# Kernel optimization log

Hardware: AMD Instinct MI355X
Metric: run time of the kernel (lower is better)

## Reference

```python
import jax, jax.numpy as jnp
import numpy as np


def setup_inputs() -> dict:
    key = jax.random.key(0)
    k1, k2, k3, k4 = jax.random.split(key, 4)
    B, Cin, Cout, H, W = 4, 256, 256, 96, 96
    x = jax.random.normal(k1, (B, Cin, H, W), dtype=jnp.float32)
    offset = jax.random.normal(k2, (B, 18, H, W), dtype=jnp.float32)
    mask = jax.random.uniform(k3, (B, 9, H, W), dtype=jnp.float32)
    weight = jax.random.normal(k4, (Cout, Cin, 3, 3), dtype=jnp.float32) * 0.05
    gamma = jnp.ones((Cout,), dtype=jnp.float32)
    beta = jnp.zeros((Cout,), dtype=jnp.float32)
    return {"x": x, "offset": offset, "mask": mask, "weight": weight, "gamma": gamma, "beta": beta}


def reference(x, offset, mask, weight, gamma, beta):
    # Modulated deformable conv v2 (3x3, stride 1, pad 1, no bias) + GroupNorm(8) + ReLU
    B, C, H, W = x.shape
    O = weight.shape[0]
    K = 9
    xh = jnp.transpose(x, (0, 2, 3, 1))  # [B,H,W,C]
    ky, kx = jnp.meshgrid(jnp.arange(3), jnp.arange(3), indexing="ij")
    ky = ky.reshape(1, K, 1, 1).astype(x.dtype)
    kx = kx.reshape(1, K, 1, 1).astype(x.dtype)
    off = offset.reshape(B, K, 2, H, W)  # (dy, dx) per kernel tap, row-major taps
    gy = jnp.arange(H, dtype=x.dtype).reshape(1, 1, H, 1)
    gx = jnp.arange(W, dtype=x.dtype).reshape(1, 1, 1, W)
    py = gy + ky - 1.0 + off[:, :, 0]  # [B,K,H,W] sampling y
    px = gx + kx - 1.0 + off[:, :, 1]  # [B,K,H,W] sampling x
    y0 = jnp.floor(py)
    x0 = jnp.floor(px)
    wy = py - y0
    wx = px - x0
    y0i = y0.astype(jnp.int32)
    x0i = x0.astype(jnp.int32)
    bidx = jnp.arange(B).reshape(B, 1, 1, 1)

    def gather(yi, xi):
        valid = ((yi >= 0) & (yi < H) & (xi >= 0) & (xi < W)).astype(x.dtype)
        v = xh[bidx, jnp.clip(yi, 0, H - 1), jnp.clip(xi, 0, W - 1)]  # [B,K,H,W,C]
        return v * valid[..., None]

    val = (gather(y0i, x0i) * ((1 - wy) * (1 - wx))[..., None]
           + gather(y0i, x0i + 1) * ((1 - wy) * wx)[..., None]
           + gather(y0i + 1, x0i) * (wy * (1 - wx))[..., None]
           + gather(y0i + 1, x0i + 1) * (wy * wx)[..., None])
    val = val * mask[..., None]  # modulation, [B,K,H,W,C]
    out = jnp.einsum("bkhwc,ock->bohw", val, weight.reshape(O, C, K))
    # GroupNorm with 8 groups, eps=1e-5 (affine)
    G = 8
    og = out.reshape(B, G, O // G, H, W)
    mu = og.mean(axis=(2, 3, 4), keepdims=True)
    var = og.var(axis=(2, 3, 4), keepdims=True)
    og = (og - mu) * jax.lax.rsqrt(var + 1e-5)
    out = og.reshape(B, O, H, W) * gamma.reshape(1, O, 1, 1) + beta.reshape(1, O, 1, 1)
    return jax.nn.relu(out)
```

## Files before the change

### kernel.cpp

```cpp
#include <hip/hip_runtime.h>
#include <hip/hip_bf16.h>
#include <stdint.h>

typedef __attribute__((ext_vector_type(4))) float f32x4;
typedef __attribute__((ext_vector_type(8))) short s16x8;
typedef __attribute__((ext_vector_type(4))) unsigned int u32x4;
typedef unsigned short u16;
typedef unsigned int u32;

#define B_ 4
#define C_ 256
#define O_ 256
#define H_ 96
#define W_ 96
#define HW_ (H_*W_)
#define M_ (B_*HW_)

static __device__ __forceinline__ float asf(u32 u){
    union { u32 u; float f; } x; x.u = u; return x.f;
}
static __device__ __forceinline__ u16 f2bf(float f){
    union { float f; u32 u; } x; x.f = f;
    u32 u = x.u;
    u32 r = (u + 0x7fffu + ((u >> 16) & 1u)) >> 16;
    return (u16)r;
}
static __device__ __forceinline__ u32 blerp_pack(u32 q00, u32 q01, u32 q10, u32 q11,
                                                 float w00, float w01, float w10, float w11)
{
    float f0 = asf(q00 << 16) * w00 + asf(q01 << 16) * w01
             + asf(q10 << 16) * w10 + asf(q11 << 16) * w11;
    float f1 = asf(q00) * w00 + asf(q01) * w01 + asf(q10) * w10 + asf(q11) * w11;
    float2 fp; fp.x = f0; fp.y = f1;
    __hip_bfloat162 hb = __float22bfloat162_rn(fp);
    union { __hip_bfloat162 h; u32 u; } cv; cv.h = hb;
    return cv.u;
}

struct TapCtx {
    float w00, w01, w10, w11;
    u32 o00, o01, o10, o11;
};

static __device__ __forceinline__ TapCtx tap_setup(
    int tap, int b, int h, int w, int hw,
    const float* __restrict__ off, const float* __restrict__ msk)
{
    TapCtx t;
    float dy = off[(size_t)(b * 18 + 2 * tap) * HW_ + hw];
    float dx = off[(size_t)(b * 18 + 2 * tap + 1) * HW_ + hw];
    float mk = msk[(size_t)(b * 9 + tap) * HW_ + hw];
    float py = (float)(h + tap / 3 - 1) + dy;
    float px = (float)(w + tap % 3 - 1) + dx;
    float fy = floorf(py), fx = floorf(px);
    float wy = py - fy, wx = px - fx;
    int y0 = (int)fy, x0 = (int)fx;
    int y1 = y0 + 1, x1 = x0 + 1;
    float w00 = (1.f - wy) * (1.f - wx) * mk;
    float w01 = (1.f - wy) * wx * mk;
    float w10 = wy * (1.f - wx) * mk;
    float w11 = wy * wx * mk;
    if (y0 < 0 || y0 >= H_) { w00 = 0.f; w01 = 0.f; }
    if (y1 < 0 || y1 >= H_) { w10 = 0.f; w11 = 0.f; }
    if (x0 < 0 || x0 >= W_) { w00 = 0.f; w10 = 0.f; }
    if (x1 < 0 || x1 >= W_) { w01 = 0.f; w11 = 0.f; }
    int cy0 = min(max(y0, 0), H_ - 1), cy1 = min(max(y1, 0), H_ - 1);
    int cx0 = min(max(x0, 0), W_ - 1), cx1 = min(max(x1, 0), W_ - 1);
    u32 rb = (u32)b * (u32)(HW_ * C_);
    t.o00 = rb + ((u32)(cy0 * W_ + cx0)) * C_;
    t.o01 = rb + ((u32)(cy0 * W_ + cx1)) * C_;
    t.o10 = rb + ((u32)(cy1 * W_ + cx0)) * C_;
    t.o11 = rb + ((u32)(cy1 * W_ + cx1)) * C_;
    t.w00 = w00; t.w01 = w01; t.w10 = w10; t.w11 = w11;
    return t;
}

__global__ __launch_bounds__(256) void transpose_x(const float* __restrict__ x,
                                                   u16* __restrict__ xT)
{
    __shared__ float t[32][33];
    int tid = threadIdx.x;
    int tx = tid & 31, ty = tid >> 5;
    int bi = blockIdx.x;
    int w0 = (bi % 3) * 32;
    int c0 = ((bi / 3) % 8) * 32;
    int bh = bi / 24;
    int b = bh / H_, h = bh - b * H_;
    #pragma unroll
    for (int r = 0; r < 4; ++r){
        int c = c0 + ty + r * 8;
        t[ty + r * 8][tx] = x[(size_t)(b * C_ + c) * HW_ + h * W_ + w0 + tx];
    }
    __syncthreads();
    #pragma unroll
    for (int r = 0; r < 4; ++r){
        int w = w0 + ty + r * 8;
        xT[((size_t)(b * H_ + h) * W_ + w) * C_ + c0 + tx] = f2bf(t[tx][ty + r * 8]);
    }
}

__global__ __launch_bounds__(256) void pack_w(const float* __restrict__ wt,
                                              u16* __restrict__ w3)
{
    int n = blockIdx.x * 256 + threadIdx.x;
    int o = n / 2304;
    int rem = n - o * 2304;
    int c = rem / 9;
    int tap = rem - c * 9;
    int kidx = tap * 256 + c;
    w3[(size_t)(kidx >> 3) * 2048 + o * 8 + (kidx & 7)] = f2bf(wt[n]);
}

__global__ __launch_bounds__(512, 4) void dcn_main(
    const float* __restrict__ off, const float* __restrict__ msk,
    const u16* __restrict__ xT, const u16* __restrict__ w3,
    float* __restrict__ convOut, float* __restrict__ stats)
{
    __shared__ u16 At[2][64 * 256];
    int tid = threadIdx.x;
    int lane = tid & 63;
    int wv = tid >> 6;
    int l15 = lane & 15;
    int g = lane >> 4;

    int bid = blockIdx.x;
    int tile = (bid & 7) * 72 + (bid >> 3);
    int b = tile / 144;
    int t = tile - b * 144;
    int ty_ = t / 12, tx_ = t - ty_ * 12;
    int py0 = ty_ * 8, px0 = tx_ * 8;

    f32x4 acc[4][2];
    #pragma unroll
    for (int i = 0; i < 4; ++i)
        #pragma unroll
        for (int q = 0; q < 2; ++q)
            acc[i][q] = (f32x4){0.f, 0.f, 0.f, 0.f};

    int p = tid >> 3;
    int k = tid & 7;
    int h = py0 + (p >> 3);
    int w = px0 + (p & 7);
    int hw = h * W_ + w;

    {
        TapCtx tp = tap_setup(0, b, h, w, hw, off, msk);
        #pragma unroll
        for (int i = 0; i < 4; ++i){
            int ck = k + i * 8;
            int c = ck * 8;
            u32x4 q00 = *(const u32x4*)(xT + tp.o00 + c);
            u32x4 q01 = *(const u32x4*)(xT + tp.o01 + c);
            u32x4 q10 = *(const u32x4*)(xT + tp.o10 + c);
            u32x4 q11 = *(const u32x4*)(xT + tp.o11 + c);
            u32x4 outv;
            #pragma unroll
            for (int j = 0; j < 4; ++j)
                outv[j] = blerp_pack(q00[j], q01[j], q10[j], q11[j],
                                     tp.w00, tp.w01, tp.w10, tp.w11);
            u32 boff = (u32)(p * 512) + (u32)((ck ^ (p & 15)) << 4);
            *(u32x4*)((char*)&At[0][0] + boff) = outv;
        }
    }
    __syncthreads();

    int cur = 0;
    for (int tap = 0; tap < 9; ++tap){
        bool pre = (tap < 8);
        TapCtx tn;
        u32x4 s00, s01, s10, s11;
        if (pre){
            tn = tap_setup(tap + 1, b, h, w, hw, off, msk);
            int c = k * 8;
            s00 = *(const u32x4*)(xT + tn.o00 + c);
            s01 = *(const u32x4*)(xT + tn.o01 + c);
            s10 = *(const u32x4*)(xT + tn.o10 + c);
            s11 = *(const u32x4*)(xT + tn.o11 + c);
        }
        const char* Ac = (const char*)&At[cur][0];
        char* An = (char*)&At[cur ^ 1][0];

        #pragma unroll
        for (int half = 0; half < 4; ++half){
            __builtin_amdgcn_s_setprio(1);
            #pragma unroll
            for (int s = 0; s < 2; ++s){
                int step = half * 2 + s;
                int ck = step * 4 + g;
                s16x8 a[4];
                #pragma unroll
                for (int i = 0; i < 4; ++i){
                    int r = i * 16 + l15;
                    u32 boff = (u32)(r * 512) + (u32)((ck ^ (r & 15)) << 4);
                    a[i] = *(const s16x8*)(Ac + boff);
                }
                const u16* wrow = w3 + (size_t)(tap * 32 + step * 4 + g) * 2048
                                + (size_t)(wv * 32 + l15) * 8;
                s16x8 b0 = *(const s16x8*)(wrow);
                s16x8 b1 = *(const s16x8*)(wrow + 128);
                #pragma unroll
                for (int i = 0; i < 4; ++i){
                    acc[i][0] = __builtin_amdgcn_mfma_f32_16x16x32_bf16(a[i], b0, acc[i][0], 0, 0, 0);
                    acc[i][1] = __builtin_amdgcn_mfma_f32_16x16x32_bf16(a[i], b1, acc[i][1], 0, 0, 0);
                }
            }
            __builtin_amdgcn_s_setprio(0);

            if (pre){
                int ck = k + half * 8;
                u32x4 outv;
                #pragma unroll
                for (int j = 0; j < 4; ++j)
                    outv[j] = blerp_pack(s00[j], s01[j], s10[j], s11[j],
                                         tn.w00, tn.w01, tn.w10, tn.w11);
                u32 boff = (u32)(p * 512) + (u32)((ck ^ (p & 15)) << 4);
                *(u32x4*)(An + boff) = outv;
                if (half < 3){
                    int c = (k + (half + 1) * 8) * 8;
                    s00 = *(const u32x4*)(xT + tn.o00 + c);
                    s01 = *(const u32x4*)(xT + tn.o01 + c);
                    s10 = *(const u32x4*)(xT + tn.o10 + c);
                    s11 = *(const u32x4*)(xT + tn.o11 + c);
                }
            }
        }
        __syncthreads();
        cur ^= 1;
    }

    float s0 = 0.f, s20 = 0.f;
    size_t mbase = (size_t)b * HW_;
    #pragma unroll
    for (int i = 0; i < 4; ++i){
        #pragma unroll
        for (int q = 0; q < 2; ++q){
            int oc = wv * 32 + q * 16 + l15;
            #pragma unroll
            for (int j = 0; j < 4; ++j){
                float v = acc[i][q][j];
                int pp = i * 16 + g * 4 + j;
                int mr_hw = (py0 + (pp >> 3)) * W_ + px0 + (pp & 7);
                convOut[(mbase + mr_hw) * 256 + oc] = v;
                s0 += v; s20 += v * v;
            }
        }
    }
    #pragma unroll
    for (int d = 32; d; d >>= 1){
        s0  += __shfl_xor(s0, d, 64);
        s20 += __shfl_xor(s20, d, 64);
    }
    if (lane == 0){
        atomicAdd(&stats[(b * 8 + wv) * 2 + 0], s0);
        atomicAdd(&stats[(b * 8 + wv) * 2 + 1], s20);
    }
}

__global__ __launch_bounds__(256) void gn_final(
    const float* __restrict__ convOut, const float* __restrict__ stats,
    const float* __restrict__ gamma, const float* __restrict__ beta,
    float* __restrict__ out)
{
    __shared__ float t[64][257];
    int tid = threadIdx.x;
    int m0 = blockIdx.x * 64;
    int b = m0 / HW_;
    const f32x4* src = (const f32x4*)(convOut + (size_t)m0 * 256);
    #pragma unroll
    for (int it = 0; it < 16; ++it){
        int idx = it * 256 + tid;
        int r = idx >> 6;
        int c4 = idx & 63;
        f32x4 v = src[(size_t)r * 64 + c4];
        t[r][c4 * 4 + 0] = v[0];
        t[r][c4 * 4 + 1] = v[1];
        t[r][c4 * 4 + 2] = v[2];
        t[r][c4 * 4 + 3] = v[3];
    }
    __syncthreads();
    int lanem = tid & 63;
    int hw = (m0 - b * HW_) + lanem;
    float* dst = out + (size_t)b * O_ * HW_ + hw;
    const float invN = 1.f / 294912.f;
    #pragma unroll 8
    for (int it = 0; it < 64; ++it){
        int o = it * 4 + (tid >> 6);
        int gidx = (b * 8 + (o >> 5)) * 2;
        float sm = stats[gidx + 0];
        float sq = stats[gidx + 1];
        float mu = sm * invN;
        float var = sq * invN - mu * mu;
        float inv = rsqrtf(var + 1e-5f);
        float sc = gamma[o] * inv;
        float sh = beta[o] - mu * sc;
        float v = t[lanem][o];
        dst[(size_t)o * HW_] = fmaxf(v * sc + sh, 0.f);
    }
}

extern "C" void kernel_launch(void* const* d_in, const int* in_sizes, int n_in,
                              void* d_out, int out_size, void* d_ws, size_t ws_size,
                              hipStream_t stream)
{
    const float* x     = (const float*)d_in[0];
    const float* off   = (const float*)d_in[1];
    const float* msk   = (const float*)d_in[2];
    const float* wt    = (const float*)d_in[3];
    const float* gamma = (const float*)d_in[4];
    const float* beta  = (const float*)d_in[5];
    float* out = (float*)d_out;

    char* ws = (char*)d_ws;
    u16*   xT      = (u16*)ws;
    u16*   w3      = (u16*)(ws + 18874368);
    float* convOut = (float*)(ws + 20054016);
    float* stats   = (float*)(ws + 57802752);

    hipMemsetAsync(stats, 0, 256, stream);
    hipLaunchKernelGGL(transpose_x, dim3(9216), dim3(256), 0, stream, x, xT);
    hipLaunchKernelGGL(pack_w,      dim3(2304), dim3(256), 0, stream, wt, w3);
    hipLaunchKernelGGL(dcn_main,    dim3(576),  dim3(512), 0, stream,
                       off, msk, xT, w3, convOut, stats);
    hipLaunchKernelGGL(gn_final,    dim3(576),  dim3(256), 0, stream,
                       convOut, stats, gamma, beta, out);
}
```

Before: 171.2 us.

## Store conv intermediate as packed bf16 and merge prep kernels

```diff
diff --git a/kernel.cpp b/kernel.cpp
--- a/kernel.cpp
+++ b/kernel.cpp
@@ -24,6 +24,9 @@
     u32 u = x.u;
     u32 r = (u + 0x7fffu + ((u >> 16) & 1u)) >> 16;
     return (u16)r;
+}
+static __device__ __forceinline__ float bf2f(u16 u){
+    union { u32 u; float f; } x; x.u = ((u32)u) << 16; return x.f;
 }
 static __device__ __forceinline__ u32 blerp_pack(u32 q00, u32 q01, u32 q10, u32 q11,
                                                  float w00, float w01, float w10, float w11)
@@ -75,13 +78,25 @@
     return t;
 }
 
-__global__ __launch_bounds__(256) void transpose_x(const float* __restrict__ x,
-                                                   u16* __restrict__ xT)
-{
+__global__ __launch_bounds__(256) void prep(const float* __restrict__ x,
+                                            const float* __restrict__ wt,
+                                            u16* __restrict__ xT,
+                                            u16* __restrict__ w3)
+{
+    int bi = blockIdx.x;
+    int tid = threadIdx.x;
+    if (bi >= 9216){
+        int n = (bi - 9216) * 256 + tid;
+        int o = n / 2304;
+        int rem = n - o * 2304;
+        int c = rem / 9;
+        int tap = rem - c * 9;
+        int kidx = tap * 256 + c;
+        w3[(size_t)(kidx >> 3) * 2048 + o * 8 + (kidx & 7)] = f2bf(wt[n]);
+        return;
+    }
     __shared__ float t[32][33];
-    int tid = threadIdx.x;
     int tx = tid & 31, ty = tid >> 5;
-    int bi = blockIdx.x;
     int w0 = (bi % 3) * 32;
     int c0 = ((bi / 3) % 8) * 32;
     int bh = bi / 24;
@@ -99,22 +114,10 @@
     }
 }
 
-__global__ __launch_bounds__(256) void pack_w(const float* __restrict__ wt,
-                                              u16* __restrict__ w3)
-{
-    int n = blockIdx.x * 256 + threadIdx.x;
-    int o = n / 2304;
-    int rem = n - o * 2304;
-    int c = rem / 9;
-    int tap = rem - c * 9;
-    int kidx = tap * 256 + c;
-    w3[(size_t)(kidx >> 3) * 2048 + o * 8 + (kidx & 7)] = f2bf(wt[n]);
-}
-
 __global__ __launch_bounds__(512, 4) void dcn_main(
     const float* __restrict__ off, const float* __restrict__ msk,
     const u16* __restrict__ xT, const u16* __restrict__ w3,
-    float* __restrict__ convOut, float* __restrict__ stats)
+    u32* __restrict__ convB, float* __restrict__ stats)
 {
     __shared__ u16 At[2][64 * 256];
     int tid = threadIdx.x;
@@ -233,16 +236,14 @@
     #pragma unroll
     for (int i = 0; i < 4; ++i){
         #pragma unroll
-        for (int q = 0; q < 2; ++q){
-            int oc = wv * 32 + q * 16 + l15;
-            #pragma unroll
-            for (int j = 0; j < 4; ++j){
-                float v = acc[i][q][j];
-                int pp = i * 16 + g * 4 + j;
-                int mr_hw = (py0 + (pp >> 3)) * W_ + px0 + (pp & 7);
-                convOut[(mbase + mr_hw) * 256 + oc] = v;
-                s0 += v; s20 += v * v;
-            }
+        for (int j = 0; j < 4; ++j){
+            float v0 = acc[i][0][j];
+            float v1 = acc[i][1][j];
+            int pp = i * 16 + g * 4 + j;
+            int mr_hw = (py0 + (pp >> 3)) * W_ + px0 + (pp & 7);
+            u32 pk = ((u32)f2bf(v1) << 16) | (u32)f2bf(v0);
+            convB[(mbase + mr_hw) * 128 + wv * 16 + l15] = pk;
+            s0 += v0 + v1; s20 += v0 * v0 + v1 * v1;
         }
     }
     #pragma unroll
@@ -257,7 +258,7 @@
 }
 
 __global__ __launch_bounds__(256) void gn_final(
-    const float* __restrict__ convOut, const float* __restrict__ stats,
+    const u32* __restrict__ convB, const float* __restrict__ stats,
     const float* __restrict__ gamma, const float* __restrict__ beta,
     float* __restrict__ out)
 {
@@ -265,17 +266,20 @@
     int tid = threadIdx.x;
     int m0 = blockIdx.x * 64;
     int b = m0 / HW_;
-    const f32x4* src = (const f32x4*)(convOut + (size_t)m0 * 256);
-    #pragma unroll
-    for (int it = 0; it < 16; ++it){
+    const u32x4* src = (const u32x4*)(convB + (size_t)m0 * 128);
+    #pragma unroll
+    for (int it = 0; it < 8; ++it){
         int idx = it * 256 + tid;
-        int r = idx >> 6;
-        int c4 = idx & 63;
-        f32x4 v = src[(size_t)r * 64 + c4];
-        t[r][c4 * 4 + 0] = v[0];
-        t[r][c4 * 4 + 1] = v[1];
-        t[r][c4 * 4 + 2] = v[2];
-        t[r][c4 * 4 + 3] = v[3];
+        int r = idx >> 5;
+        int c4 = idx & 31;
+        u32x4 v = src[(size_t)r * 32 + c4];
+        #pragma unroll
+        for (int jj = 0; jj < 4; ++jj){
+            int pos = c4 * 4 + jj;
+            int o_lo = ((pos >> 4) << 5) + (pos & 15);
+            t[r][o_lo]      = bf2f((u16)(v[jj] & 0xffff));
+            t[r][o_lo + 16] = bf2f((u16)(v[jj] >> 16));
+        }
     }
     __syncthreads();
     int lanem = tid & 63;
@@ -311,16 +315,15 @@
     float* out = (float*)d_out;
 
     char* ws = (char*)d_ws;
-    u16*   xT      = (u16*)ws;
-    u16*   w3      = (u16*)(ws + 18874368);
-    float* convOut = (float*)(ws + 20054016);
-    float* stats   = (float*)(ws + 57802752);
+    u16*   xT    = (u16*)ws;
+    u16*   w3    = (u16*)(ws + 18874368);
+    u32*   convB = (u32*)(ws + 20054016);
+    float* stats = (float*)(ws + 57802752);
 
     hipMemsetAsync(stats, 0, 256, stream);
-    hipLaunchKernelGGL(transpose_x, dim3(9216), dim3(256), 0, stream, x, xT);
-    hipLaunchKernelGGL(pack_w,      dim3(2304), dim3(256), 0, stream, wt, w3);
-    hipLaunchKernelGGL(dcn_main,    dim3(576),  dim3(512), 0, stream,
-                       off, msk, xT, w3, convOut, stats);
-    hipLaunchKernelGGL(gn_final,    dim3(576),  dim3(256), 0, stream,
-                       convOut, stats, gamma, beta, out);
-}
+    hipLaunchKernelGGL(prep,     dim3(11520), dim3(256), 0, stream, x, wt, xT, w3);
+    hipLaunchKernelGGL(dcn_main, dim3(576),   dim3(512), 0, stream,
+                       off, msk, xT, w3, convB, stats);
+    hipLaunchKernelGGL(gn_final, dim3(576),   dim3(256), 0, stream,
+                       convB, stats, gamma, beta, out);
+}
```

New measurement: 167.1 us. 1.02x faster.
